# Kernel tuning notes

Measured on AMD Instinct MI355X. Metric: run time of the kernel, lower is better.

## Reference

```python
import jax, jax.numpy as jnp
import numpy as np

EMB = 384
H = 6
D = 64
B = 256
T = 256


def setup_inputs() -> dict:
    key = jax.random.key(0)
    ks = jax.random.split(key, 6)
    s = 1.0 / np.sqrt(EMB)
    return {
        "x": jax.random.normal(ks[0], (B, T, EMB), dtype=jnp.float32),
        "wq": jax.random.normal(ks[1], (H, EMB, D), dtype=jnp.float32) * s,
        "wk": jax.random.normal(ks[2], (H, EMB, D), dtype=jnp.float32) * s,
        "wv": jax.random.normal(ks[3], (H, EMB, D), dtype=jnp.float32) * s,
        "w_proj": jax.random.normal(ks[4], (H * D, EMB), dtype=jnp.float32) * s,
        "b_proj": jax.random.normal(ks[5], (EMB,), dtype=jnp.float32) * 0.01,
    }


def reference(x, wq, wk, wv, w_proj, b_proj):
    # x: [B, T, E]; per-head projections stacked over H (dropout in eval mode)
    q = jnp.einsum("bte,hed->bhtd", x, wq)
    k = jnp.einsum("bte,hed->bhtd", x, wk)
    v = jnp.einsum("bte,hed->bhtd", x, wv)
    scale = q.shape[-1] ** -0.5
    scores = jnp.einsum("bhqd,bhkd->bhqk", q, k) * scale  # [B,H,T,T]
    tq = q.shape[2]
    causal = jnp.tril(jnp.ones((tq, tq), dtype=bool))
    scores = jnp.where(causal, scores, -jnp.inf)
    att = jax.nn.softmax(scores, axis=-1)
    out = jnp.einsum("bhqk,bhkd->bhqd", att, v)  # [B,H,T,D]
    out = out.transpose(0, 2, 1, 3).reshape(x.shape[0], tq, -1)  # concat heads
    return out @ w_proj + b_proj
```

## Files before the change

### kernel.cpp

```cpp
#include <hip/hip_runtime.h>
#include <hip/hip_bf16.h>


#define Bn 256
#define Tn 256
#define En 384
#define Hn 6
#define Dn 64

typedef __bf16 bf16x8 __attribute__((ext_vector_type(8)));
typedef float f32x4 __attribute__((ext_vector_type(4)));
typedef unsigned short u16x8 __attribute__((ext_vector_type(8)));

static __device__ __forceinline__ unsigned short f2bf(float f) {
    unsigned int u = __builtin_bit_cast(unsigned int, f);
    u += 0x7fffu + ((u >> 16) & 1u);
    return (unsigned short)(u >> 16);
}

static __device__ __forceinline__ f32x4 mfma16(bf16x8 a, bf16x8 b, f32x4 c) {
    return __builtin_amdgcn_mfma_f32_16x16x32_bf16(a, b, c, 0, 0, 0);
}

__global__ __launch_bounds__(256) void prep_kernel(
    const float* __restrict__ wq, const float* __restrict__ wk,
    const float* __restrict__ wv, const float* __restrict__ wp,
    unsigned short* __restrict__ wt, unsigned short* __restrict__ wpt) {
    const int NW = 3 * Hn * Dn * En;
    const int NP = En * En;
    int idx = blockIdx.x * 256 + threadIdx.x;
    if (idx < NW) {
        int e = idx % En;
        int d = (idx / En) % Dn;
        int h = (idx / (En * Dn)) % Hn;
        int t = idx / (En * Dn * Hn);
        const float* src = (t == 0) ? wq : (t == 1) ? wk : wv;
        wt[idx] = f2bf(src[(h * En + e) * Dn + d]);
    } else if (idx < NW + NP) {
        int j = idx - NW;
        int k = j % En;
        int n = j / En;
        wpt[j] = f2bf(wp[k * En + n]);
    }
}

__global__ __launch_bounds__(256) void xcast_kernel(
    const float* __restrict__ x, unsigned short* __restrict__ xb) {
    size_t i = ((size_t)blockIdx.x * 256 + threadIdx.x) * 8;
    float4 f0 = *(const float4*)(x + i);
    float4 f1 = *(const float4*)(x + i + 4);
    u16x8 p;
    p[0] = f2bf(f0.x); p[1] = f2bf(f0.y); p[2] = f2bf(f0.z); p[3] = f2bf(f0.w);
    p[4] = f2bf(f1.x); p[5] = f2bf(f1.y); p[6] = f2bf(f1.z); p[7] = f2bf(f1.w);
    *(u16x8*)(xb + i) = p;
}

__global__ __launch_bounds__(256) void qkv_gemm(
    const unsigned short* __restrict__ xb, const unsigned short* __restrict__ wt,
    unsigned short* __restrict__ Qo, unsigned short* __restrict__ Ko,
    unsigned short* __restrict__ Vt) {
    __shared__ unsigned short As[128][72];
    __shared__ unsigned short Bs[192][72];

    const int m0 = blockIdx.x * 128;
    const int h = blockIdx.y;

    const int tid = threadIdx.x;
    const int wave = tid >> 6, lane = tid & 63;
    const int quad = lane >> 4, l16 = lane & 15;
    const int mw = (wave >> 1) * 64, nw = (wave & 1) * 96;

    f32x4 acc[4][6];
#pragma unroll
    for (int i = 0; i < 4; ++i)
#pragma unroll
        for (int j = 0; j < 6; ++j) acc[i][j] = (f32x4){0.f, 0.f, 0.f, 0.f};

    const int ar = tid >> 1, ac0 = (tid & 1) * 32;
    const unsigned short* wrow = wt + (size_t)(((tid >> 6) * Hn + h) * Dn + (tid & 63)) * En;

    for (int kb = 0; kb < 6; ++kb) {
        const int k0 = kb * 64;
        const unsigned short* xr = xb + (size_t)(m0 + ar) * En + k0 + ac0;
#pragma unroll
        for (int i = 0; i < 4; ++i)
            *(uint4*)&As[ar][ac0 + i * 8] = *(const uint4*)(xr + i * 8);
        if (tid < 192) {
            const unsigned short* wr = wrow + k0;
#pragma unroll
            for (int i = 0; i < 8; ++i)
                *(uint4*)&Bs[tid][i * 8] = *(const uint4*)(wr + i * 8);
        }
        __syncthreads();
#pragma unroll
        for (int ks = 0; ks < 2; ++ks) {
            bf16x8 a[4], b[6];
#pragma unroll
            for (int mi = 0; mi < 4; ++mi)
                a[mi] = *(const bf16x8*)&As[mw + mi * 16 + l16][ks * 32 + quad * 8];
#pragma unroll
            for (int ni = 0; ni < 6; ++ni)
                b[ni] = *(const bf16x8*)&Bs[nw + ni * 16 + l16][ks * 32 + quad * 8];
#pragma unroll
            for (int mi = 0; mi < 4; ++mi)
#pragma unroll
                for (int ni = 0; ni < 6; ++ni) acc[mi][ni] = mfma16(a[mi], b[ni], acc[mi][ni]);
        }
        __syncthreads();
    }

    const int b = m0 >> 8, tbase = m0 & 255;
    unsigned short* qkbase[2] = {
        Qo + (size_t)((b * Hn + h) * Tn) * Dn,
        Ko + (size_t)((b * Hn + h) * Tn) * Dn };
    unsigned short* vdst = Vt + (size_t)((b * Hn + h) * Dn) * Tn;
#pragma unroll
    for (int ni = 0; ni < 6; ++ni) {
        const int ng = nw + ni * 16;
        const int tensor = ng >> 6;
        const int d = (ng & 63) + l16;
        if (tensor < 2) {
            unsigned short* dst = qkbase[tensor];
#pragma unroll
            for (int mi = 0; mi < 4; ++mi)
#pragma unroll
                for (int r = 0; r < 4; ++r) {
                    int t = tbase + mw + mi * 16 + quad * 4 + r;
                    dst[t * Dn + d] = f2bf(acc[mi][ni][r]);
                }
        } else {
#pragma unroll
            for (int mi = 0; mi < 4; ++mi) {
                int t0 = tbase + mw + mi * 16 + quad * 4;
                ushort4 pk;
                pk.x = f2bf(acc[mi][ni][0]);
                pk.y = f2bf(acc[mi][ni][1]);
                pk.z = f2bf(acc[mi][ni][2]);
                pk.w = f2bf(acc[mi][ni][3]);
                *(ushort4*)&vdst[d * Tn + t0] = pk;
            }
        }
    }
}

__global__ __launch_bounds__(256) void attn_kernel(
    const unsigned short* __restrict__ Q, const unsigned short* __restrict__ K,
    const unsigned short* __restrict__ Vt, unsigned short* __restrict__ attout) {
    __shared__ unsigned short Kt[64][72];
    __shared__ unsigned short Vl[64][72];
    __shared__ unsigned short P[64][72];

    const int qt = blockIdx.x, h = blockIdx.y, b = blockIdx.z;
    const int q0 = qt * 64;
    const unsigned short* Qb = Q + (size_t)((b * Hn + h) * Tn) * Dn;
    const unsigned short* Kb = K + (size_t)((b * Hn + h) * Tn) * Dn;
    const unsigned short* Vb = Vt + (size_t)((b * Hn + h) * Dn) * Tn;

    const int tid = threadIdx.x;
    const int wave = tid >> 6, lane = tid & 63;
    const int quad = lane >> 4, l16 = lane & 15;

    bf16x8 aq[2];
#pragma unroll
    for (int ks = 0; ks < 2; ++ks)
        aq[ks] = *(const bf16x8*)&Qb[(q0 + wave * 16 + l16) * Dn + ks * 32 + quad * 8];

    f32x4 O[4];
#pragma unroll
    for (int i = 0; i < 4; ++i) O[i] = (f32x4){0.f, 0.f, 0.f, 0.f};
    float rsum[4] = {0.f, 0.f, 0.f, 0.f};

    const int sr = tid >> 2, sc = (tid & 3) * 16;
    const int qrow_base = q0 + wave * 16 + quad * 4;
    const float cexp = 0.125f * 1.44269504f;

#pragma unroll
    for (int kt = 0; kt < 4; ++kt) {
        if (kt <= qt) {
            __syncthreads();
            const unsigned short* kr = Kb + (kt * 64 + sr) * Dn + sc;
            *(uint4*)&Kt[sr][sc] = *(const uint4*)kr;
            *(uint4*)&Kt[sr][sc + 8] = *(const uint4*)(kr + 8);
            const unsigned short* vr = Vb + sr * Tn + kt * 64 + sc;
            *(uint4*)&Vl[sr][sc] = *(const uint4*)vr;
            *(uint4*)&Vl[sr][sc + 8] = *(const uint4*)(vr + 8);
            __syncthreads();

            f32x4 S[4];
#pragma unroll
            for (int i = 0; i < 4; ++i) S[i] = (f32x4){0.f, 0.f, 0.f, 0.f};
#pragma unroll
            for (int ks = 0; ks < 2; ++ks)
#pragma unroll
                for (int ni = 0; ni < 4; ++ni) {
                    bf16x8 bk = *(const bf16x8*)&Kt[ni * 16 + l16][ks * 32 + quad * 8];
                    S[ni] = mfma16(aq[ks], bk, S[ni]);
                }

#pragma unroll
            for (int ni = 0; ni < 4; ++ni)
#pragma unroll
                for (int r = 0; r < 4; ++r) {
                    int col = kt * 64 + ni * 16 + l16;
                    float p = exp2f(S[ni][r] * cexp);
                    p = (col > qrow_base + r) ? 0.f : p;
                    rsum[r] += p;
                    P[wave * 16 + quad * 4 + r][ni * 16 + l16] = f2bf(p);
                }

#pragma unroll
            for (int ks = 0; ks < 2; ++ks) {
                bf16x8 ap = *(const bf16x8*)&P[wave * 16 + l16][ks * 32 + quad * 8];
#pragma unroll
                for (int ni = 0; ni < 4; ++ni) {
                    bf16x8 bv = *(const bf16x8*)&Vl[ni * 16 + l16][ks * 32 + quad * 8];
                    O[ni] = mfma16(ap, bv, O[ni]);
                }
            }
        }
    }

#pragma unroll
    for (int r = 0; r < 4; ++r) {
        float s = rsum[r];
        s += __shfl_xor(s, 1);
        s += __shfl_xor(s, 2);
        s += __shfl_xor(s, 4);
        s += __shfl_xor(s, 8);
        rsum[r] = s;
    }

    __syncthreads();
#pragma unroll
    for (int r = 0; r < 4; ++r) {
        float inv = 1.0f / rsum[r];
#pragma unroll
        for (int ni = 0; ni < 4; ++ni)
            Kt[wave * 16 + quad * 4 + r][ni * 16 + l16] = f2bf(O[ni][r] * inv);
    }
    __syncthreads();
    const int row = tid >> 2;
    const int col = (tid & 3) * 16;
    unsigned short* dst = attout + (size_t)(b * Tn + q0 + row) * (Hn * Dn) + h * Dn + col;
    *(uint4*)dst = *(const uint4*)&Kt[row][col];
    *(uint4*)(dst + 8) = *(const uint4*)&Kt[row][col + 8];
}

__global__ __launch_bounds__(256) void proj_gemm(
    const unsigned short* __restrict__ attout, const unsigned short* __restrict__ wpt,
    const float* __restrict__ bproj, float* __restrict__ out) {
    __shared__ unsigned short As[128][72];
    __shared__ unsigned short Bs[128][72];

    const int m0 = blockIdx.x * 128;
    const int n0 = blockIdx.y * 128;

    const int tid = threadIdx.x;
    const int wave = tid >> 6, lane = tid & 63;
    const int quad = lane >> 4, l16 = lane & 15;
    const int mw = (wave >> 1) * 64, nw = (wave & 1) * 64;

    f32x4 acc[4][4];
#pragma unroll
    for (int i = 0; i < 4; ++i)
#pragma unroll
        for (int j = 0; j < 4; ++j) acc[i][j] = (f32x4){0.f, 0.f, 0.f, 0.f};

    const int ar = tid >> 1, ac0 = (tid & 1) * 32;

    for (int kb = 0; kb < 6; ++kb) {
        const int k0 = kb * 64;
        const unsigned short* am = attout + (size_t)(m0 + ar) * En + k0 + ac0;
#pragma unroll
        for (int i = 0; i < 4; ++i)
            *(uint4*)&As[ar][ac0 + i * 8] = *(const uint4*)(am + i * 8);
        const unsigned short* wr = wpt + (size_t)(n0 + ar) * En + k0 + ac0;
#pragma unroll
        for (int i = 0; i < 4; ++i)
            *(uint4*)&Bs[ar][ac0 + i * 8] = *(const uint4*)(wr + i * 8);
        __syncthreads();
#pragma unroll
        for (int ks = 0; ks < 2; ++ks) {
            bf16x8 a[4], bb[4];
#pragma unroll
            for (int mi = 0; mi < 4; ++mi)
                a[mi] = *(const bf16x8*)&As[mw + mi * 16 + l16][ks * 32 + quad * 8];
#pragma unroll
            for (int ni = 0; ni < 4; ++ni)
                bb[ni] = *(const bf16x8*)&Bs[nw + ni * 16 + l16][ks * 32 + quad * 8];
#pragma unroll
            for (int mi = 0; mi < 4; ++mi)
#pragma unroll
                for (int ni = 0; ni < 4; ++ni) acc[mi][ni] = mfma16(a[mi], bb[ni], acc[mi][ni]);
        }
        __syncthreads();
    }
#pragma unroll
    for (int mi = 0; mi < 4; ++mi)
#pragma unroll
        for (int ni = 0; ni < 4; ++ni)
#pragma unroll
            for (int r = 0; r < 4; ++r) {
                int row = m0 + mw + mi * 16 + quad * 4 + r;
                int col = n0 + nw + ni * 16 + l16;
                out[(size_t)row * En + col] = acc[mi][ni][r] + bproj[col];
            }
}

extern "C" void kernel_launch(void* const* d_in, const int* in_sizes, int n_in,
                              void* d_out, int out_size, void* d_ws, size_t ws_size,
                              hipStream_t stream) {
    const float* x  = (const float*)d_in[0];
    const float* wq = (const float*)d_in[1];
    const float* wk = (const float*)d_in[2];
    const float* wv = (const float*)d_in[3];
    const float* wp = (const float*)d_in[4];
    const float* bp = (const float*)d_in[5];
    float* out = (float*)d_out;

    char* ws = (char*)d_ws;
    const size_t WT_OFF  = 0;
    const size_t WPT_OFF = WT_OFF + 884736;
    const size_t Q_OFF   = WPT_OFF + 294912;
    const size_t K_OFF   = Q_OFF + 50331648ull;
    const size_t VT_OFF  = K_OFF + 50331648ull;
    const size_t XB_OFF  = VT_OFF + 50331648ull;

    unsigned short* wt   = (unsigned short*)(ws + WT_OFF);
    unsigned short* wpt  = (unsigned short*)(ws + WPT_OFF);
    unsigned short* Qd   = (unsigned short*)(ws + Q_OFF);
    unsigned short* Kd   = (unsigned short*)(ws + K_OFF);
    unsigned short* Vtd  = (unsigned short*)(ws + VT_OFF);
    unsigned short* xbd  = (unsigned short*)(ws + XB_OFF);
    unsigned short* ao   = xbd;

    prep_kernel<<<2304, 256, 0, stream>>>(wq, wk, wv, wp, wt, wpt);
    xcast_kernel<<<12288, 256, 0, stream>>>(x, xbd);
    qkv_gemm<<<dim3(512, Hn), 256, 0, stream>>>(xbd, wt, Qd, Kd, Vtd);
    attn_kernel<<<dim3(4, Hn, Bn), 256, 0, stream>>>(Qd, Kd, Vtd, ao);
    proj_gemm<<<dim3(512, 3), 256, 0, stream>>>(ao, wpt, bp, out);
}
```

Baseline: 410.8 us.

## Prefetch next tile into registers during MFMA compute in all three kernels

Adds register-level software pipelining to the QKV projection GEMM, the attention kernel and the output projection GEMM. The next K-tile's global loads are issued into registers right after the shared-memory barrier, so they overlap the current tile's MFMA work instead of stalling before it. This costs extra VGPRs for the staged tiles (up to 12 uint4 per thread in the QKV GEMM), which could lower occupancy. The attention loop also becomes a runtime-bounded loop over kt ≤ qt instead of an unrolled loop with a guard.

After: 627.8 us. 1.53x slower.

```diff
diff --git a/kernel.cpp b/kernel.cpp
--- a/kernel.cpp
+++ b/kernel.cpp
@@ -78,20 +78,38 @@
 
     const int ar = tid >> 1, ac0 = (tid & 1) * 32;
     const unsigned short* wrow = wt + (size_t)(((tid >> 6) * Hn + h) * Dn + (tid & 63)) * En;
+    const unsigned short* xrow = xb + (size_t)(m0 + ar) * En + ac0;
+
+    uint4 ra[4];
+    uint4 rb[8];
+#pragma unroll
+    for (int i = 0; i < 4; ++i) ra[i] = *(const uint4*)(xrow + i * 8);
+    if (tid < 192) {
+#pragma unroll
+        for (int i = 0; i < 8; ++i) rb[i] = *(const uint4*)(wrow + i * 8);
+    }
 
     for (int kb = 0; kb < 6; ++kb) {
-        const int k0 = kb * 64;
-        const unsigned short* xr = xb + (size_t)(m0 + ar) * En + k0 + ac0;
-#pragma unroll
-        for (int i = 0; i < 4; ++i)
-            *(uint4*)&As[ar][ac0 + i * 8] = *(const uint4*)(xr + i * 8);
+#pragma unroll
+        for (int i = 0; i < 4; ++i) *(uint4*)&As[ar][ac0 + i * 8] = ra[i];
         if (tid < 192) {
-            const unsigned short* wr = wrow + k0;
-#pragma unroll
-            for (int i = 0; i < 8; ++i)
-                *(uint4*)&Bs[tid][i * 8] = *(const uint4*)(wr + i * 8);
-        }
-        __syncthreads();
+#pragma unroll
+            for (int i = 0; i < 8; ++i) *(uint4*)&Bs[tid][i * 8] = rb[i];
+        }
+        __syncthreads();
+
+        if (kb < 5) {
+            const int k0 = (kb + 1) * 64;
+            const unsigned short* xr = xrow + k0;
+#pragma unroll
+            for (int i = 0; i < 4; ++i) ra[i] = *(const uint4*)(xr + i * 8);
+            if (tid < 192) {
+                const unsigned short* wr = wrow + k0;
+#pragma unroll
+                for (int i = 0; i < 8; ++i) rb[i] = *(const uint4*)(wr + i * 8);
+            }
+        }
+
 #pragma unroll
         for (int ks = 0; ks < 2; ++ks) {
             bf16x8 a[4], b[6];
@@ -174,48 +192,59 @@
     const int qrow_base = q0 + wave * 16 + quad * 4;
     const float cexp = 0.125f * 1.44269504f;
 
-#pragma unroll
-    for (int kt = 0; kt < 4; ++kt) {
-        if (kt <= qt) {
-            __syncthreads();
-            const unsigned short* kr = Kb + (kt * 64 + sr) * Dn + sc;
-            *(uint4*)&Kt[sr][sc] = *(const uint4*)kr;
-            *(uint4*)&Kt[sr][sc + 8] = *(const uint4*)(kr + 8);
-            const unsigned short* vr = Vb + sr * Tn + kt * 64 + sc;
-            *(uint4*)&Vl[sr][sc] = *(const uint4*)vr;
-            *(uint4*)&Vl[sr][sc + 8] = *(const uint4*)(vr + 8);
-            __syncthreads();
-
-            f32x4 S[4];
-#pragma unroll
-            for (int i = 0; i < 4; ++i) S[i] = (f32x4){0.f, 0.f, 0.f, 0.f};
-#pragma unroll
-            for (int ks = 0; ks < 2; ++ks)
-#pragma unroll
-                for (int ni = 0; ni < 4; ++ni) {
-                    bf16x8 bk = *(const bf16x8*)&Kt[ni * 16 + l16][ks * 32 + quad * 8];
-                    S[ni] = mfma16(aq[ks], bk, S[ni]);
-                }
-
-#pragma unroll
-            for (int ni = 0; ni < 4; ++ni)
-#pragma unroll
-                for (int r = 0; r < 4; ++r) {
-                    int col = kt * 64 + ni * 16 + l16;
-                    float p = exp2f(S[ni][r] * cexp);
-                    p = (col > qrow_base + r) ? 0.f : p;
-                    rsum[r] += p;
-                    P[wave * 16 + quad * 4 + r][ni * 16 + l16] = f2bf(p);
-                }
-
-#pragma unroll
-            for (int ks = 0; ks < 2; ++ks) {
-                bf16x8 ap = *(const bf16x8*)&P[wave * 16 + l16][ks * 32 + quad * 8];
-#pragma unroll
-                for (int ni = 0; ni < 4; ++ni) {
-                    bf16x8 bv = *(const bf16x8*)&Vl[ni * 16 + l16][ks * 32 + quad * 8];
-                    O[ni] = mfma16(ap, bv, O[ni]);
-                }
+    const unsigned short* kr0 = Kb + sr * Dn + sc;
+    uint4 rk0 = *(const uint4*)kr0;
+    uint4 rk1 = *(const uint4*)(kr0 + 8);
+    const unsigned short* vr0 = Vb + sr * Tn + sc;
+    uint4 rv0 = *(const uint4*)vr0;
+    uint4 rv1 = *(const uint4*)(vr0 + 8);
+
+    for (int kt = 0; kt <= qt; ++kt) {
+        __syncthreads();
+        *(uint4*)&Kt[sr][sc]     = rk0;
+        *(uint4*)&Kt[sr][sc + 8] = rk1;
+        *(uint4*)&Vl[sr][sc]     = rv0;
+        *(uint4*)&Vl[sr][sc + 8] = rv1;
+        __syncthreads();
+
+        if (kt < qt) {
+            const unsigned short* kr = Kb + ((kt + 1) * 64 + sr) * Dn + sc;
+            rk0 = *(const uint4*)kr;
+            rk1 = *(const uint4*)(kr + 8);
+            const unsigned short* vr = Vb + sr * Tn + (kt + 1) * 64 + sc;
+            rv0 = *(const uint4*)vr;
+            rv1 = *(const uint4*)(vr + 8);
+        }
+
+        f32x4 S[4];
+#pragma unroll
+        for (int i = 0; i < 4; ++i) S[i] = (f32x4){0.f, 0.f, 0.f, 0.f};
+#pragma unroll
+        for (int ks = 0; ks < 2; ++ks)
+#pragma unroll
+            for (int ni = 0; ni < 4; ++ni) {
+                bf16x8 bk = *(const bf16x8*)&Kt[ni * 16 + l16][ks * 32 + quad * 8];
+                S[ni] = mfma16(aq[ks], bk, S[ni]);
+            }
+
+#pragma unroll
+        for (int ni = 0; ni < 4; ++ni)
+#pragma unroll
+            for (int r = 0; r < 4; ++r) {
+                int col = kt * 64 + ni * 16 + l16;
+                float p = exp2f(S[ni][r] * cexp);
+                p = (col > qrow_base + r) ? 0.f : p;
+                rsum[r] += p;
+                P[wave * 16 + quad * 4 + r][ni * 16 + l16] = f2bf(p);
+            }
+
+#pragma unroll
+        for (int ks = 0; ks < 2; ++ks) {
+            bf16x8 ap = *(const bf16x8*)&P[wave * 16 + l16][ks * 32 + quad * 8];
+#pragma unroll
+            for (int ni = 0; ni < 4; ++ni) {
+                bf16x8 bv = *(const bf16x8*)&Vl[ni * 16 + l16][ks * 32 + quad * 8];
+                O[ni] = mfma16(ap, bv, O[ni]);
             }
         }
     }
@@ -267,18 +296,30 @@
         for (int j = 0; j < 4; ++j) acc[i][j] = (f32x4){0.f, 0.f, 0.f, 0.f};
 
     const int ar = tid >> 1, ac0 = (tid & 1) * 32;
+    const unsigned short* arow = attout + (size_t)(m0 + ar) * En + ac0;
+    const unsigned short* brow = wpt + (size_t)(n0 + ar) * En + ac0;
+
+    uint4 ra[4], rw[4];
+#pragma unroll
+    for (int i = 0; i < 4; ++i) ra[i] = *(const uint4*)(arow + i * 8);
+#pragma unroll
+    for (int i = 0; i < 4; ++i) rw[i] = *(const uint4*)(brow + i * 8);
 
     for (int kb = 0; kb < 6; ++kb) {
-        const int k0 = kb * 64;
-        const unsigned short* am = attout + (size_t)(m0 + ar) * En + k0 + ac0;
-#pragma unroll
-        for (int i = 0; i < 4; ++i)
-            *(uint4*)&As[ar][ac0 + i * 8] = *(const uint4*)(am + i * 8);
-        const unsigned short* wr = wpt + (size_t)(n0 + ar) * En + k0 + ac0;
-#pragma unroll
-        for (int i = 0; i < 4; ++i)
-            *(uint4*)&Bs[ar][ac0 + i * 8] = *(const uint4*)(wr + i * 8);
-        __syncthreads();
+#pragma unroll
+        for (int i = 0; i < 4; ++i) *(uint4*)&As[ar][ac0 + i * 8] = ra[i];
+#pragma unroll
+        for (int i = 0; i < 4; ++i) *(uint4*)&Bs[ar][ac0 + i * 8] = rw[i];
+        __syncthreads();
+
+        if (kb < 5) {
+            const int k0 = (kb + 1) * 64;
+#pragma unroll
+            for (int i = 0; i < 4; ++i) ra[i] = *(const uint4*)(arow + k0 + i * 8);
+#pragma unroll
+            for (int i = 0; i < 4; ++i) rw[i] = *(const uint4*)(brow + k0 + i * 8);
+        }
+
 #pragma unroll
         for (int ks = 0; ks < 2; ++ks) {
             bf16x8 a[4], bb[4];
```

## Double-buffer GEMM tiles via direct global-to-LDS loads with XOR swizzle

Applied to the files above, without the earlier changes.

Both the QKV and output-projection GEMMs now stage tiles with global_load_lds (direct global-to-LDS DMA) into double-buffered shared memory. The next K-slice is prefetched while the current one is multiplied, and the per-iteration syncs drop to one. Padding is replaced by an XOR swizzle to avoid LDS bank conflicts, and the grid is reordered so blocks sharing the same x/A rows launch adjacently, for better L2 reuse. This doubles LDS use, which may reduce occupancy, and relies on the direct-to-LDS lane ordering matching the swizzle layout.

Result: faster. 387.3 us (-5.7%).

```diff
diff --git a/kernel.cpp b/kernel.cpp
--- a/kernel.cpp
+++ b/kernel.cpp
@@ -20,6 +20,12 @@
 
 static __device__ __forceinline__ f32x4 mfma16(bf16x8 a, bf16x8 b, f32x4 c) {
     return __builtin_amdgcn_mfma_f32_16x16x32_bf16(a, b, c, 0, 0, 0);
+}
+
+static __device__ __forceinline__ void glds16(const unsigned short* g, unsigned short* l) {
+    __builtin_amdgcn_global_load_lds(
+        (const __attribute__((address_space(1))) unsigned int*)g,
+        (__attribute__((address_space(3))) unsigned int*)l, 16, 0, 0);
 }
 
 __global__ __launch_bounds__(256) void prep_kernel(
@@ -59,11 +65,11 @@
     const unsigned short* __restrict__ xb, const unsigned short* __restrict__ wt,
     unsigned short* __restrict__ Qo, unsigned short* __restrict__ Ko,
     unsigned short* __restrict__ Vt) {
-    __shared__ unsigned short As[128][72];
-    __shared__ unsigned short Bs[192][72];
-
-    const int m0 = blockIdx.x * 128;
-    const int h = blockIdx.y;
+    __shared__ unsigned short As[2][128][64];
+    __shared__ unsigned short Bs[2][192][64];
+
+    const int h = blockIdx.x;
+    const int m0 = blockIdx.y * 128;
 
     const int tid = threadIdx.x;
     const int wave = tid >> 6, lane = tid & 63;
@@ -76,38 +82,56 @@
 #pragma unroll
         for (int j = 0; j < 6; ++j) acc[i][j] = (f32x4){0.f, 0.f, 0.f, 0.f};
 
-    const int ar = tid >> 1, ac0 = (tid & 1) * 32;
-    const unsigned short* wrow = wt + (size_t)(((tid >> 6) * Hn + h) * Dn + (tid & 63)) * En;
-
+    const int lr = lane >> 3;
+    const int js = (lane & 7) ^ lr;
+
+    const unsigned short* ga[4];
+#pragma unroll
+    for (int i = 0; i < 4; ++i)
+        ga[i] = xb + (size_t)(m0 + wave * 32 + i * 8 + lr) * En + js * 8;
+    const unsigned short* gb[6];
+#pragma unroll
+    for (int i = 0; i < 6; ++i) {
+        int n = wave * 48 + i * 8 + lr;
+        gb[i] = wt + (size_t)(((n >> 6) * Hn + h) * Dn + (n & 63)) * En + js * 8;
+    }
+
+#define QKV_STAGE(buf, koff)                                              \
+    do {                                                                  \
+        _Pragma("unroll") for (int i = 0; i < 4; ++i)                     \
+            glds16(ga[i] + (koff), &As[buf][wave * 32 + i * 8][0]);       \
+        _Pragma("unroll") for (int i = 0; i < 6; ++i)                     \
+            glds16(gb[i] + (koff), &Bs[buf][wave * 48 + i * 8][0]);       \
+    } while (0)
+
+    QKV_STAGE(0, 0);
+    __syncthreads();
+
+    int cur = 0;
     for (int kb = 0; kb < 6; ++kb) {
-        const int k0 = kb * 64;
-        const unsigned short* xr = xb + (size_t)(m0 + ar) * En + k0 + ac0;
-#pragma unroll
-        for (int i = 0; i < 4; ++i)
-            *(uint4*)&As[ar][ac0 + i * 8] = *(const uint4*)(xr + i * 8);
-        if (tid < 192) {
-            const unsigned short* wr = wrow + k0;
-#pragma unroll
-            for (int i = 0; i < 8; ++i)
-                *(uint4*)&Bs[tid][i * 8] = *(const uint4*)(wr + i * 8);
-        }
-        __syncthreads();
+        if (kb < 5) QKV_STAGE(cur ^ 1, (kb + 1) * 64);
+
 #pragma unroll
         for (int ks = 0; ks < 2; ++ks) {
             bf16x8 a[4], b[6];
-#pragma unroll
-            for (int mi = 0; mi < 4; ++mi)
-                a[mi] = *(const bf16x8*)&As[mw + mi * 16 + l16][ks * 32 + quad * 8];
+            const int ps = ((ks * 4 + quad) ^ (l16 & 7)) * 8;
+#pragma unroll
+            for (int mi = 0; mi < 4; ++mi)
+                a[mi] = *(const bf16x8*)&As[cur][mw + mi * 16 + l16][ps];
 #pragma unroll
             for (int ni = 0; ni < 6; ++ni)
-                b[ni] = *(const bf16x8*)&Bs[nw + ni * 16 + l16][ks * 32 + quad * 8];
+                b[ni] = *(const bf16x8*)&Bs[cur][nw + ni * 16 + l16][ps];
 #pragma unroll
             for (int mi = 0; mi < 4; ++mi)
 #pragma unroll
                 for (int ni = 0; ni < 6; ++ni) acc[mi][ni] = mfma16(a[mi], b[ni], acc[mi][ni]);
         }
-        __syncthreads();
-    }
+        if (kb < 5) {
+            __syncthreads();
+            cur ^= 1;
+        }
+    }
+#undef QKV_STAGE
 
     const int b = m0 >> 8, tbase = m0 & 255;
     unsigned short* qkbase[2] = {
@@ -249,11 +273,11 @@
 __global__ __launch_bounds__(256) void proj_gemm(
     const unsigned short* __restrict__ attout, const unsigned short* __restrict__ wpt,
     const float* __restrict__ bproj, float* __restrict__ out) {
-    __shared__ unsigned short As[128][72];
-    __shared__ unsigned short Bs[128][72];
-
-    const int m0 = blockIdx.x * 128;
-    const int n0 = blockIdx.y * 128;
+    __shared__ unsigned short As[2][128][64];
+    __shared__ unsigned short Bs[2][128][64];
+
+    const int n0 = blockIdx.x * 128;
+    const int m0 = blockIdx.y * 128;
 
     const int tid = threadIdx.x;
     const int wave = tid >> 6, lane = tid & 63;
@@ -266,35 +290,54 @@
 #pragma unroll
         for (int j = 0; j < 4; ++j) acc[i][j] = (f32x4){0.f, 0.f, 0.f, 0.f};
 
-    const int ar = tid >> 1, ac0 = (tid & 1) * 32;
-
+    const int lr = lane >> 3;
+    const int js = (lane & 7) ^ lr;
+
+    const unsigned short* ga[4];
+    const unsigned short* gb[4];
+#pragma unroll
+    for (int i = 0; i < 4; ++i) {
+        ga[i] = attout + (size_t)(m0 + wave * 32 + i * 8 + lr) * En + js * 8;
+        gb[i] = wpt + (size_t)(n0 + wave * 32 + i * 8 + lr) * En + js * 8;
+    }
+
+#define PROJ_STAGE(buf, koff)                                             \
+    do {                                                                  \
+        _Pragma("unroll") for (int i = 0; i < 4; ++i)                     \
+            glds16(ga[i] + (koff), &As[buf][wave * 32 + i * 8][0]);       \
+        _Pragma("unroll") for (int i = 0; i < 4; ++i)                     \
+            glds16(gb[i] + (koff), &Bs[buf][wave * 32 + i * 8][0]);       \
+    } while (0)
+
+    PROJ_STAGE(0, 0);
+    __syncthreads();
+
+    int cur = 0;
     for (int kb = 0; kb < 6; ++kb) {
-        const int k0 = kb * 64;
-        const unsigned short* am = attout + (size_t)(m0 + ar) * En + k0 + ac0;
-#pragma unroll
-        for (int i = 0; i < 4; ++i)
-            *(uint4*)&As[ar][ac0 + i * 8] = *(const uint4*)(am + i * 8);
-        const unsigned short* wr = wpt + (size_t)(n0 + ar) * En + k0 + ac0;
-#pragma unroll
-        for (int i = 0; i < 4; ++i)
-            *(uint4*)&Bs[ar][ac0 + i * 8] = *(const uint4*)(wr + i * 8);
-        __syncthreads();
+        if (kb < 5) PROJ_STAGE(cur ^ 1, (kb + 1) * 64);
+
 #pragma unroll
         for (int ks = 0; ks < 2; ++ks) {
             bf16x8 a[4], bb[4];
-#pragma unroll
-            for (int mi = 0; mi < 4; ++mi)
-                a[mi] = *(const bf16x8*)&As[mw + mi * 16 + l16][ks * 32 + quad * 8];
+            const int ps = ((ks * 4 + quad) ^ (l16 & 7)) * 8;
+#pragma unroll
+            for (int mi = 0; mi < 4; ++mi)
+                a[mi] = *(const bf16x8*)&As[cur][mw + mi * 16 + l16][ps];
 #pragma unroll
             for (int ni = 0; ni < 4; ++ni)
-                bb[ni] = *(const bf16x8*)&Bs[nw + ni * 16 + l16][ks * 32 + quad * 8];
+                bb[ni] = *(const bf16x8*)&Bs[cur][nw + ni * 16 + l16][ps];
 #pragma unroll
             for (int mi = 0; mi < 4; ++mi)
 #pragma unroll
                 for (int ni = 0; ni < 4; ++ni) acc[mi][ni] = mfma16(a[mi], bb[ni], acc[mi][ni]);
         }
-        __syncthreads();
-    }
+        if (kb < 5) {
+            __syncthreads();
+            cur ^= 1;
+        }
+    }
+#undef PROJ_STAGE
+
 #pragma unroll
     for (int mi = 0; mi < 4; ++mi)
 #pragma unroll
@@ -336,7 +379,7 @@
 
     prep_kernel<<<2304, 256, 0, stream>>>(wq, wk, wv, wp, wt, wpt);
     xcast_kernel<<<12288, 256, 0, stream>>>(x, xbd);
-    qkv_gemm<<<dim3(512, Hn), 256, 0, stream>>>(xbd, wt, Qd, Kd, Vtd);
+    qkv_gemm<<<dim3(Hn, 512), 256, 0, stream>>>(xbd, wt, Qd, Kd, Vtd);
     attn_kernel<<<dim3(4, Hn, Bn), 256, 0, stream>>>(Qd, Kd, Vtd, ao);
-    proj_gemm<<<dim3(512, 3), 256, 0, stream>>>(ao, wpt, bp, out);
-}
+    proj_gemm<<<dim3(3, 512), 256, 0, stream>>>(ao, wpt, bp, out);
+}
```
